# Kernel optimization log

Hardware: AMD Instinct MI355X
Metric: run time of the kernel (lower is better)

The kernel has to match this reference:

```python
import jax, jax.numpy as jnp
import numpy as np

C, V, B, ITERS = 144, 576, 1024, 3  # checks, variables, batch, decoding iterations
COL_W = 4  # variable-node degree (ones per column of H)


def _make_H():
    """Deterministic sparse 0/1 parity-check matrix, col weight COL_W, row weight >= 2."""
    rng = np.random.default_rng(0)
    H = np.zeros((C, V), np.float32)
    for v in range(V):
        H[rng.choice(C, size=COL_W, replace=False), v] = 1.0
    for c in range(C):
        while H[c].sum() < 2:
            H[c, rng.integers(V)] = 1.0
    return H


def setup_inputs() -> dict:
    key = jax.random.key(0)
    r = jax.random.normal(key, (B, V), dtype=jnp.float32)  # channel LLRs, batched
    alpha = 0.7 * jnp.ones((ITERS,), dtype=jnp.float32)    # nn.Parameter init
    H = jnp.asarray(_make_H())                             # [C, V] 0/1 mask
    return {"r": r, "alpha": alpha, "H": H}


def _c_to_v(M, edge, a):
    """Check-to-variable min-sum messages, vectorized over batch and rows.

    For each edge (c,v): E[c,v] = a * (prod of signs of M[c, edges(c)\\{v}])
                                   * (min of |M[c, edges(c)\\{v}]|)
    Implemented with the standard two-smallest-values trick.
    """
    inf = jnp.float32(jnp.inf)
    absM = jnp.where(edge, jnp.abs(M), inf)                 # [B,C,V]
    min1 = jnp.min(absM, axis=-1, keepdims=True)            # smallest |M| per row
    idx = jnp.argmin(absM, axis=-1)                         # [B,C] its position
    is_min = jnp.arange(V)[None, None, :] == idx[..., None]  # one-hot of argmin
    min2 = jnp.min(jnp.where(is_min, inf, absM), axis=-1, keepdims=True)
    excl_min = jnp.where(is_min, min2, min1)                # min excluding self
    sgn = jnp.where(edge, jnp.sign(M), 1.0)
    row_sign = jnp.prod(sgn, axis=-1, keepdims=True)
    sgn_excl = row_sign * sgn                               # product excluding self (signs are +/-1)
    return jnp.where(edge, a * sgn_excl * excl_min, 0.0)


def reference(r, alpha, H):
    edge = (H == 1.0)[None, :, :]                           # [1,C,V] broadcast to batch
    rB = r[:, None, :]                                      # [B,1,V]
    M = jnp.where(edge, rB, 0.0)                            # initial_M: M[c,v]=r[v] on edges
    E = jnp.zeros_like(M)
    for i in range(alpha.shape[0]):
        E = _c_to_v(M, edge, alpha[i])
        col = jnp.sum(E, axis=1, keepdims=True)             # [B,1,V] sum over checks
        M = jnp.where(edge, col - E + rB, 0.0)              # update_M: extrinsic sum + r[v]
    return r + jnp.sum(E, axis=1)                           # [B,V] output LLRs
```

## Files before the change

### kernel.cpp

```cpp
#include <hip/hip_runtime.h>
#include <stdint.h>

#define CN 144
#define VN 576
#define BN 1024
#define NITER 3
#define RCAP 40
#define CCAP 8
#define TPB 192

#define WS_RLEN 0
#define WS_LOC  192
#define WS_CSC  (192 + VN*CN)
#define WS_CCNT (WS_CSC + CCAP*VN)

__device__ __forceinline__ int edge_id(int l, int c) {
    return (((l >> 2) * CN + c) << 2) | (l & 3);
}

__global__ __launch_bounds__(64) void build_stage(const float* __restrict__ H,
                                                  int* __restrict__ ws) {
    const int c = blockIdx.x;
    const int lane = threadIdx.x;
    int base = 0;
    const float* row = H + c * VN;
    for (int ch = 0; ch < VN / 64; ++ch) {
        const int v = ch * 64 + lane;
        const bool set = row[v] > 0.5f;
        const unsigned long long mask = __ballot(set);
        const int off = base + (int)__popcll(mask & ((1ULL << lane) - 1ULL));
        ws[WS_LOC + v * CN + c] = set ? off : -1;
        base += (int)__popcll(mask);
    }
    if (lane == 0) ws[WS_RLEN + c] = base;
}

__global__ __launch_bounds__(64) void build_csc(int* __restrict__ ws) {
    const int v = blockIdx.x;
    const int lane = threadIdx.x;
    int cnt = 0;
    for (int ch = 0; ch < 3; ++ch) {
        const int c = ch * 64 + lane;
        const int l = (c < CN) ? ws[WS_LOC + v * CN + c] : -1;
        const bool set = (l >= 0) && (l < RCAP);
        const unsigned long long mask = __ballot(set);
        const int off = cnt + (int)__popcll(mask & ((1ULL << lane) - 1ULL));
        if (set && off < CCAP) ws[WS_CSC + off * VN + v] = edge_id(l, c);
        cnt += (int)__popcll(mask);
    }
    if (cnt > CCAP) cnt = CCAP;
    if (lane == 0) ws[WS_CCNT + v] = cnt;
    if (lane >= cnt && lane < CCAP) ws[WS_CSC + lane * VN + v] = 0;
}

__global__ __launch_bounds__(TPB) void ldpc_decode(const float* __restrict__ r,
                                                   const float* __restrict__ alpha,
                                                   const int* __restrict__ ws,
                                                   float* __restrict__ out) {
    __shared__ float4 M4[(RCAP / 4) * CN];
    float* const Mf = reinterpret_cast<float*>(M4);

    const int b = blockIdx.x;
    const int t = threadIdx.x;
    const float a_[NITER] = { alpha[0], alpha[1], alpha[2] };

    int   ent4[3][4], entX[3][4];
    int   cnt[3];
    float rv[3];
    #pragma unroll
    for (int q = 0; q < 3; ++q) {
        const int v = t + q * TPB;
        rv[q]  = r[b * VN + v];
        cnt[q] = ws[WS_CCNT + v];
        #pragma unroll
        for (int j = 0; j < 4; ++j) ent4[q][j] = ws[WS_CSC + j * VN + v];
    }
    const int rl = (t < CN) ? ws[WS_RLEN + t] : 0;
    const int any_hi = __syncthreads_or((cnt[0] > 4) | (cnt[1] > 4) | (cnt[2] > 4));
    if (any_hi) {
        #pragma unroll
        for (int q = 0; q < 3; ++q)
            #pragma unroll
            for (int j = 0; j < 4; ++j) entX[q][j] = ws[WS_CSC + (4 + j) * VN + t + q * TPB];
    }

    if (t < CN) {
        const int rpad = (rl + 3) & ~3;
        for (int k = rl; k < rpad; ++k) Mf[edge_id(k, t)] = INFINITY;
    }
    #pragma unroll
    for (int q = 0; q < 3; ++q) {
        #pragma unroll
        for (int j = 0; j < 4; ++j) if (j < cnt[q]) Mf[ent4[q][j]] = rv[q];
    }
    if (any_hi) {
        #pragma unroll
        for (int q = 0; q < 3; ++q) {
            #pragma unroll
            for (int j = 0; j < 4; ++j) if (4 + j < cnt[q]) Mf[entX[q][j]] = rv[q];
        }
    }
    __syncthreads();

    #pragma unroll
    for (int it = 0; it < NITER; ++it) {
        const float a = a_[it];

        if (t < CN) {
            uint32_t m1 = 0x7fffffffu, m2 = 0x7fffffffu, sg = 0u;
            int am = -1;
            const int nq = (rl + 3) >> 2;
            for (int q4 = 0; q4 < nq; ++q4) {
                const float4 mv = M4[q4 * CN + t];
                const float* mvp = reinterpret_cast<const float*>(&mv);
                #pragma unroll
                for (int j = 0; j < 4; ++j) {
                    const uint32_t mb = __float_as_uint(mvp[j]);
                    const uint32_t ab = mb & 0x7fffffffu;
                    sg ^= mb;
                    const bool lt = ab < m1;
                    const uint32_t mn2 = (m2 < ab) ? m2 : ab;
                    m2 = lt ? m1 : mn2;
                    m1 = lt ? ab : m1;
                    am = lt ? (q4 * 4 + j) : am;
                }
            }
            sg &= 0x80000000u;
            const uint32_t p1b = __float_as_uint(a * __uint_as_float(m1)) ^ sg;
            const uint32_t p2b = __float_as_uint(a * __uint_as_float(m2)) ^ sg;

            const int nqf = rl >> 2;
            for (int q4 = 0; q4 < nqf; ++q4) {
                const float4 mv = M4[q4 * CN + t];
                const float* mvp = reinterpret_cast<const float*>(&mv);
                float ev[4];
                #pragma unroll
                for (int j = 0; j < 4; ++j) {
                    const uint32_t mb = __float_as_uint(mvp[j]);
                    const uint32_t ps = ((q4 * 4 + j) == am) ? p2b : p1b;
                    ev[j] = __uint_as_float(ps ^ (mb & 0x80000000u));
                }
                M4[q4 * CN + t] = make_float4(ev[0], ev[1], ev[2], ev[3]);
            }
            if (rl & 3) {
                const int q4 = nqf;
                const float4 mv = M4[q4 * CN + t];
                const float* mvp = reinterpret_cast<const float*>(&mv);
                float ev[4];
                #pragma unroll
                for (int j = 0; j < 4; ++j) {
                    const int k = q4 * 4 + j;
                    const uint32_t mb = __float_as_uint(mvp[j]);
                    const uint32_t ps = (k == am) ? p2b : p1b;
                    ev[j] = (k < rl) ? __uint_as_float(ps ^ (mb & 0x80000000u)) : mvp[j];
                }
                M4[q4 * CN + t] = make_float4(ev[0], ev[1], ev[2], ev[3]);
            }
        }
        __syncthreads();

        #pragma unroll
        for (int q = 0; q < 3; ++q) {
            float E4[4], EX[4];
            float col = 0.0f;
            #pragma unroll
            for (int j = 0; j < 4; ++j) {
                E4[j] = (j < cnt[q]) ? Mf[ent4[q][j]] : 0.0f;
                col += E4[j];
            }
            if (any_hi) {
                #pragma unroll
                for (int j = 0; j < 4; ++j) {
                    EX[j] = (4 + j < cnt[q]) ? Mf[entX[q][j]] : 0.0f;
                    col += EX[j];
                }
            }
            if (it == NITER - 1) {
                out[b * VN + t + q * TPB] = rv[q] + col;
            } else {
                const float mb = col + rv[q];
                #pragma unroll
                for (int j = 0; j < 4; ++j) if (j < cnt[q]) Mf[ent4[q][j]] = mb - E4[j];
                if (any_hi) {
                    #pragma unroll
                    for (int j = 0; j < 4; ++j) if (4 + j < cnt[q]) Mf[entX[q][j]] = mb - EX[j];
                }
            }
        }
        if (it < NITER - 1) __syncthreads();
    }
}

extern "C" void kernel_launch(void* const* d_in, const int* in_sizes, int n_in,
                              void* d_out, int out_size, void* d_ws, size_t ws_size,
                              hipStream_t stream) {
    const float* r     = (const float*)d_in[0];
    const float* alpha = (const float*)d_in[1];
    const float* H     = (const float*)d_in[2];
    float* out = (float*)d_out;
    int* ws    = (int*)d_ws;

    build_stage<<<CN, 64, 0, stream>>>(H, ws);
    build_csc<<<VN, 64, 0, stream>>>(ws);
    ldpc_decode<<<BN, TPB, 0, stream>>>(r, alpha, ws, out);
}
```

Before: 24.86 us.

## Sort check rows by degree, vectorize CSC loads, cache row messages in registers

The last block of build_stage to finish, chosen through an atomic counter, sorts check rows by row length so that adjacent threads in a wavefront have similar loop trip counts. This is meant to reduce divergence in the check-node pass. The CSC edge table is repacked per variable as int4 so each thread reads its entries with one vector load. The check-node pass now keeps the row's float4 messages in registers instead of reading shared memory twice, at the cost of more registers and a fully unrolled, predicated loop.

```diff
diff --git a/kernel.cpp b/kernel.cpp
--- a/kernel.cpp
+++ b/kernel.cpp
@@ -6,33 +6,74 @@
 #define BN 1024
 #define NITER 3
 #define RCAP 40
+#define NQ   (RCAP/4)
 #define CCAP 8
 #define TPB 192
 
 #define WS_RLEN 0
-#define WS_LOC  192
-#define WS_CSC  (192 + VN*CN)
-#define WS_CCNT (WS_CSC + CCAP*VN)
-
-__device__ __forceinline__ int edge_id(int l, int c) {
-    return (((l >> 2) * CN + c) << 2) | (l & 3);
-}
-
-__global__ __launch_bounds__(64) void build_stage(const float* __restrict__ H,
-                                                  int* __restrict__ ws) {
+#define WS_CTR  144
+#define WS_CCOF 160
+#define WS_RLR  304
+#define WS_CCNT 448
+#define WS_LOC  1024
+#define WS_CSC2 (1024 + CN*VN)
+#define WS_CSX  (WS_CSC2 + VN*4)
+
+__device__ __forceinline__ int edge_id(int l, int cc) {
+    return (((l >> 2) * CN + cc) << 2) | (l & 3);
+}
+
+__global__ __launch_bounds__(192) void build_stage(const float* __restrict__ H,
+                                                   int* __restrict__ ws) {
+    __shared__ int rls[CN];
+    __shared__ int hist[RCAP + 1];
+    __shared__ int pfx[RCAP + 1];
+    __shared__ int iswin;
     const int c = blockIdx.x;
-    const int lane = threadIdx.x;
-    int base = 0;
-    const float* row = H + c * VN;
-    for (int ch = 0; ch < VN / 64; ++ch) {
-        const int v = ch * 64 + lane;
-        const bool set = row[v] > 0.5f;
-        const unsigned long long mask = __ballot(set);
-        const int off = base + (int)__popcll(mask & ((1ULL << lane) - 1ULL));
-        ws[WS_LOC + v * CN + c] = set ? off : -1;
-        base += (int)__popcll(mask);
-    }
-    if (lane == 0) ws[WS_RLEN + c] = base;
+    const int t = threadIdx.x;
+
+    if (t < 64) {
+        int base = 0;
+        const float* row = H + c * VN;
+        for (int ch = 0; ch < VN / 64; ++ch) {
+            const int v = ch * 64 + t;
+            const bool set = row[v] > 0.5f;
+            const unsigned long long mask = __ballot(set);
+            const int off = base + (int)__popcll(mask & ((1ULL << t) - 1ULL));
+            ws[WS_LOC + v * CN + c] = set ? off : -1;
+            base += (int)__popcll(mask);
+        }
+        if (t == 0) ws[WS_RLEN + c] = base;
+    }
+    if (t == 0) {
+        __threadfence();
+        const unsigned old = atomicAdd((unsigned*)(ws + WS_CTR), 1u);
+        iswin = ((old % (unsigned)CN) == (unsigned)(CN - 1)) ? 1 : 0;
+    }
+    __syncthreads();
+    if (!iswin) return;
+    __threadfence();
+
+    if (t < CN)
+        rls[t] = min(__hip_atomic_load(ws + WS_RLEN + t, __ATOMIC_RELAXED,
+                                       __HIP_MEMORY_SCOPE_AGENT), RCAP);
+    if (t <= RCAP) hist[t] = 0;
+    __syncthreads();
+    if (t < CN) atomicAdd(&hist[rls[t]], 1);
+    __syncthreads();
+    if (t == 0) {
+        int acc = 0;
+        for (int i = 0; i <= RCAP; ++i) { pfx[i] = acc; acc += hist[i]; }
+    }
+    __syncthreads();
+    if (t < CN) {
+        const int key = rls[t];
+        int tie = 0;
+        for (int c2 = 0; c2 < t; ++c2) tie += (rls[c2] == key) ? 1 : 0;
+        const int cc = pfx[key] + tie;
+        ws[WS_CCOF + t] = cc;
+        ws[WS_RLR + cc] = key;
+    }
 }
 
 __global__ __launch_bounds__(64) void build_csc(int* __restrict__ ws) {
@@ -45,19 +86,25 @@
         const bool set = (l >= 0) && (l < RCAP);
         const unsigned long long mask = __ballot(set);
         const int off = cnt + (int)__popcll(mask & ((1ULL << lane) - 1ULL));
-        if (set && off < CCAP) ws[WS_CSC + off * VN + v] = edge_id(l, c);
+        if (set && off < CCAP) {
+            const int cc = ws[WS_CCOF + c];
+            const int e = edge_id(l, cc);
+            if (off < 4) ws[WS_CSC2 + v * 4 + off] = e;
+            else         ws[WS_CSX  + v * 4 + (off - 4)] = e;
+        }
         cnt += (int)__popcll(mask);
     }
     if (cnt > CCAP) cnt = CCAP;
     if (lane == 0) ws[WS_CCNT + v] = cnt;
-    if (lane >= cnt && lane < CCAP) ws[WS_CSC + lane * VN + v] = 0;
+    if (lane < 4 && lane >= cnt)     ws[WS_CSC2 + v * 4 + lane] = 0;
+    if (lane < 4 && lane + 4 >= cnt) ws[WS_CSX  + v * 4 + lane] = 0;
 }
 
 __global__ __launch_bounds__(TPB) void ldpc_decode(const float* __restrict__ r,
                                                    const float* __restrict__ alpha,
                                                    const int* __restrict__ ws,
                                                    float* __restrict__ out) {
-    __shared__ float4 M4[(RCAP / 4) * CN];
+    __shared__ float4 M4[NQ * CN];
     float* const Mf = reinterpret_cast<float*>(M4);
 
     const int b = blockIdx.x;
@@ -72,16 +119,17 @@
         const int v = t + q * TPB;
         rv[q]  = r[b * VN + v];
         cnt[q] = ws[WS_CCNT + v];
-        #pragma unroll
-        for (int j = 0; j < 4; ++j) ent4[q][j] = ws[WS_CSC + j * VN + v];
-    }
-    const int rl = (t < CN) ? ws[WS_RLEN + t] : 0;
+        const int4 e4 = *reinterpret_cast<const int4*>(ws + WS_CSC2 + v * 4);
+        ent4[q][0] = e4.x; ent4[q][1] = e4.y; ent4[q][2] = e4.z; ent4[q][3] = e4.w;
+    }
+    const int rl = (t < CN) ? ws[WS_RLR + t] : 0;
     const int any_hi = __syncthreads_or((cnt[0] > 4) | (cnt[1] > 4) | (cnt[2] > 4));
     if (any_hi) {
         #pragma unroll
-        for (int q = 0; q < 3; ++q)
-            #pragma unroll
-            for (int j = 0; j < 4; ++j) entX[q][j] = ws[WS_CSC + (4 + j) * VN + t + q * TPB];
+        for (int q = 0; q < 3; ++q) {
+            const int4 e4 = *reinterpret_cast<const int4*>(ws + WS_CSX + (t + q * TPB) * 4);
+            entX[q][0] = e4.x; entX[q][1] = e4.y; entX[q][2] = e4.z; entX[q][3] = e4.w;
+        }
     }
 
     if (t < CN) {
@@ -107,54 +155,46 @@
         const float a = a_[it];
 
         if (t < CN) {
+            const int nq = (rl + 3) >> 2;
+            float4 mv[NQ];
             uint32_t m1 = 0x7fffffffu, m2 = 0x7fffffffu, sg = 0u;
-            int am = -1;
-            const int nq = (rl + 3) >> 2;
-            for (int q4 = 0; q4 < nq; ++q4) {
-                const float4 mv = M4[q4 * CN + t];
-                const float* mvp = reinterpret_cast<const float*>(&mv);
-                #pragma unroll
-                for (int j = 0; j < 4; ++j) {
-                    const uint32_t mb = __float_as_uint(mvp[j]);
-                    const uint32_t ab = mb & 0x7fffffffu;
-                    sg ^= mb;
-                    const bool lt = ab < m1;
-                    const uint32_t mn2 = (m2 < ab) ? m2 : ab;
-                    m2 = lt ? m1 : mn2;
-                    m1 = lt ? ab : m1;
-                    am = lt ? (q4 * 4 + j) : am;
+            int am = 0;
+            #pragma unroll
+            for (int q4 = 0; q4 < NQ; ++q4) {
+                if (q4 < nq) {
+                    mv[q4] = M4[q4 * CN + t];
+                    const float* mp = reinterpret_cast<const float*>(&mv[q4]);
+                    #pragma unroll
+                    for (int j = 0; j < 4; ++j) {
+                        const uint32_t mb = __float_as_uint(mp[j]);
+                        const uint32_t ab = mb & 0x7fffffffu;
+                        sg ^= mb;
+                        const bool lt = ab < m1;
+                        m2 = lt ? m1 : ((ab < m2) ? ab : m2);
+                        m1 = lt ? ab : m1;
+                        am = lt ? (q4 * 4 + j) : am;
+                    }
                 }
             }
             sg &= 0x80000000u;
             const uint32_t p1b = __float_as_uint(a * __uint_as_float(m1)) ^ sg;
             const uint32_t p2b = __float_as_uint(a * __uint_as_float(m2)) ^ sg;
-
-            const int nqf = rl >> 2;
-            for (int q4 = 0; q4 < nqf; ++q4) {
-                const float4 mv = M4[q4 * CN + t];
-                const float* mvp = reinterpret_cast<const float*>(&mv);
-                float ev[4];
-                #pragma unroll
-                for (int j = 0; j < 4; ++j) {
-                    const uint32_t mb = __float_as_uint(mvp[j]);
-                    const uint32_t ps = ((q4 * 4 + j) == am) ? p2b : p1b;
-                    ev[j] = __uint_as_float(ps ^ (mb & 0x80000000u));
-                }
-                M4[q4 * CN + t] = make_float4(ev[0], ev[1], ev[2], ev[3]);
-            }
-            if (rl & 3) {
-                const int q4 = nqf;
-                const float4 mv = M4[q4 * CN + t];
-                const float* mvp = reinterpret_cast<const float*>(&mv);
-                float ev[4];
-                #pragma unroll
-                for (int j = 0; j < 4; ++j) {
-                    const int k = q4 * 4 + j;
-                    const uint32_t mb = __float_as_uint(mvp[j]);
-                    const uint32_t ps = (k == am) ? p2b : p1b;
-                    ev[j] = (k < rl) ? __uint_as_float(ps ^ (mb & 0x80000000u)) : mvp[j];
-                }
-                M4[q4 * CN + t] = make_float4(ev[0], ev[1], ev[2], ev[3]);
+            #pragma unroll
+            for (int q4 = 0; q4 < NQ; ++q4) {
+                if (q4 < nq) {
+                    const float* mp = reinterpret_cast<const float*>(&mv[q4]);
+                    float4 ev;
+                    float* ep = reinterpret_cast<float*>(&ev);
+                    #pragma unroll
+                    for (int j = 0; j < 4; ++j) {
+                        const int k = q4 * 4 + j;
+                        const uint32_t mb = __float_as_uint(mp[j]);
+                        const uint32_t ps = (k == am) ? p2b : p1b;
+                        ep[j] = (k < rl) ? __uint_as_float(ps ^ (mb & 0x80000000u))
+                                         : mp[j];
+                    }
+                    M4[q4 * CN + t] = ev;
+                }
             }
         }
         __syncthreads();
@@ -200,7 +240,7 @@
     float* out = (float*)d_out;
     int* ws    = (int*)d_ws;
 
-    build_stage<<<CN, 64, 0, stream>>>(H, ws);
+    build_stage<<<CN, 192, 0, stream>>>(H, ws);
     build_csc<<<VN, 64, 0, stream>>>(ws);
     ldpc_decode<<<BN, TPB, 0, stream>>>(r, alpha, ws, out);
 }
```

After: 28.48 us. 1.15x slower.

## Process four batch elements per block with float4-interleaved edge messages

Applied to the files above, without the earlier changes.

Each block now decodes four batch rows at once. Each shared-memory float4 holds one edge's messages for the four batch elements, where before it held four consecutive edges of one row. This removes the padding and tail handling and spreads the per-edge index and degree setup over four samples. The cost is 4x shared memory per block (RCAP*CN float4), 4x fewer blocks (256), and RCAP lowered to 32, which could truncate rows with more than 32 edges.

```diff
diff --git a/kernel.cpp b/kernel.cpp
--- a/kernel.cpp
+++ b/kernel.cpp
@@ -5,18 +5,17 @@
 #define VN 576
 #define BN 1024
 #define NITER 3
-#define RCAP 40
+#define RCAP 32
 #define CCAP 8
 #define TPB 192
+#define BPB 4
 
 #define WS_RLEN 0
 #define WS_LOC  192
-#define WS_CSC  (192 + VN*CN)
+#define WS_CSC  (192 + CN*VN)
 #define WS_CCNT (WS_CSC + CCAP*VN)
 
-__device__ __forceinline__ int edge_id(int l, int c) {
-    return (((l >> 2) * CN + c) << 2) | (l & 3);
-}
+union F4 { float4 v; float f[4]; uint32_t u[4]; };
 
 __global__ __launch_bounds__(64) void build_stage(const float* __restrict__ H,
                                                   int* __restrict__ ws) {
@@ -45,7 +44,7 @@
         const bool set = (l >= 0) && (l < RCAP);
         const unsigned long long mask = __ballot(set);
         const int off = cnt + (int)__popcll(mask & ((1ULL << lane) - 1ULL));
-        if (set && off < CCAP) ws[WS_CSC + off * VN + v] = edge_id(l, c);
+        if (set && off < CCAP) ws[WS_CSC + off * VN + v] = l * CN + c;
         cnt += (int)__popcll(mask);
     }
     if (cnt > CCAP) cnt = CCAP;
@@ -53,29 +52,29 @@
     if (lane >= cnt && lane < CCAP) ws[WS_CSC + lane * VN + v] = 0;
 }
 
-__global__ __launch_bounds__(TPB) void ldpc_decode(const float* __restrict__ r,
-                                                   const float* __restrict__ alpha,
-                                                   const int* __restrict__ ws,
-                                                   float* __restrict__ out) {
-    __shared__ float4 M4[(RCAP / 4) * CN];
-    float* const Mf = reinterpret_cast<float*>(M4);
+__global__ __launch_bounds__(TPB) void ldpc_decode4(const float* __restrict__ r,
+                                                    const float* __restrict__ alpha,
+                                                    const int* __restrict__ ws,
+                                                    float* __restrict__ out) {
+    __shared__ float4 M4[RCAP * CN];
 
-    const int b = blockIdx.x;
+    const int b4 = blockIdx.x * BPB;
     const int t = threadIdx.x;
     const float a_[NITER] = { alpha[0], alpha[1], alpha[2] };
 
-    int   ent4[3][4], entX[3][4];
-    int   cnt[3];
-    float rv[3];
+    int ent4[3][4], entX[3][4];
+    int cnt[3];
+    F4  rv[3];
     #pragma unroll
     for (int q = 0; q < 3; ++q) {
         const int v = t + q * TPB;
-        rv[q]  = r[b * VN + v];
+        #pragma unroll
+        for (int s = 0; s < BPB; ++s) rv[q].f[s] = r[(b4 + s) * VN + v];
         cnt[q] = ws[WS_CCNT + v];
         #pragma unroll
         for (int j = 0; j < 4; ++j) ent4[q][j] = ws[WS_CSC + j * VN + v];
     }
-    const int rl = (t < CN) ? ws[WS_RLEN + t] : 0;
+    const int rl = (t < CN) ? min(ws[WS_RLEN + t], RCAP) : 0;
     const int any_hi = __syncthreads_or((cnt[0] > 4) | (cnt[1] > 4) | (cnt[2] > 4));
     if (any_hi) {
         #pragma unroll
@@ -84,20 +83,16 @@
             for (int j = 0; j < 4; ++j) entX[q][j] = ws[WS_CSC + (4 + j) * VN + t + q * TPB];
     }
 
-    if (t < CN) {
-        const int rpad = (rl + 3) & ~3;
-        for (int k = rl; k < rpad; ++k) Mf[edge_id(k, t)] = INFINITY;
-    }
     #pragma unroll
     for (int q = 0; q < 3; ++q) {
         #pragma unroll
-        for (int j = 0; j < 4; ++j) if (j < cnt[q]) Mf[ent4[q][j]] = rv[q];
+        for (int j = 0; j < 4; ++j) if (j < cnt[q]) M4[ent4[q][j]] = rv[q].v;
     }
     if (any_hi) {
         #pragma unroll
         for (int q = 0; q < 3; ++q) {
             #pragma unroll
-            for (int j = 0; j < 4; ++j) if (4 + j < cnt[q]) Mf[entX[q][j]] = rv[q];
+            for (int j = 0; j < 4; ++j) if (4 + j < cnt[q]) M4[entX[q][j]] = rv[q].v;
         }
     }
     __syncthreads();
@@ -107,83 +102,73 @@
         const float a = a_[it];
 
         if (t < CN) {
-            uint32_t m1 = 0x7fffffffu, m2 = 0x7fffffffu, sg = 0u;
-            int am = -1;
-            const int nq = (rl + 3) >> 2;
-            for (int q4 = 0; q4 < nq; ++q4) {
-                const float4 mv = M4[q4 * CN + t];
-                const float* mvp = reinterpret_cast<const float*>(&mv);
+            uint32_t m1[BPB], m2[BPB], sg[BPB]; int am[BPB];
+            #pragma unroll
+            for (int s = 0; s < BPB; ++s) { m1[s] = 0x7fffffffu; m2[s] = 0x7fffffffu; sg[s] = 0u; am[s] = 0; }
+            for (int l = 0; l < rl; ++l) {
+                F4 mv; mv.v = M4[l * CN + t];
                 #pragma unroll
-                for (int j = 0; j < 4; ++j) {
-                    const uint32_t mb = __float_as_uint(mvp[j]);
+                for (int s = 0; s < BPB; ++s) {
+                    const uint32_t mb = mv.u[s];
                     const uint32_t ab = mb & 0x7fffffffu;
-                    sg ^= mb;
-                    const bool lt = ab < m1;
-                    const uint32_t mn2 = (m2 < ab) ? m2 : ab;
-                    m2 = lt ? m1 : mn2;
-                    m1 = lt ? ab : m1;
-                    am = lt ? (q4 * 4 + j) : am;
+                    sg[s] ^= mb;
+                    const bool lt = ab < m1[s];
+                    m2[s] = lt ? m1[s] : ((ab < m2[s]) ? ab : m2[s]);
+                    m1[s] = lt ? ab : m1[s];
+                    am[s] = lt ? l : am[s];
                 }
             }
-            sg &= 0x80000000u;
-            const uint32_t p1b = __float_as_uint(a * __uint_as_float(m1)) ^ sg;
-            const uint32_t p2b = __float_as_uint(a * __uint_as_float(m2)) ^ sg;
-
-            const int nqf = rl >> 2;
-            for (int q4 = 0; q4 < nqf; ++q4) {
-                const float4 mv = M4[q4 * CN + t];
-                const float* mvp = reinterpret_cast<const float*>(&mv);
-                float ev[4];
+            uint32_t p1b[BPB], p2b[BPB];
+            #pragma unroll
+            for (int s = 0; s < BPB; ++s) {
+                const uint32_t sgn = sg[s] & 0x80000000u;
+                p1b[s] = __float_as_uint(a * __uint_as_float(m1[s])) ^ sgn;
+                p2b[s] = __float_as_uint(a * __uint_as_float(m2[s])) ^ sgn;
+            }
+            for (int l = 0; l < rl; ++l) {
+                F4 mv; mv.v = M4[l * CN + t];
+                F4 ev;
                 #pragma unroll
-                for (int j = 0; j < 4; ++j) {
-                    const uint32_t mb = __float_as_uint(mvp[j]);
-                    const uint32_t ps = ((q4 * 4 + j) == am) ? p2b : p1b;
-                    ev[j] = __uint_as_float(ps ^ (mb & 0x80000000u));
+                for (int s = 0; s < BPB; ++s) {
+                    const uint32_t ps = (l == am[s]) ? p2b[s] : p1b[s];
+                    ev.u[s] = ps ^ (mv.u[s] & 0x80000000u);
                 }
-                M4[q4 * CN + t] = make_float4(ev[0], ev[1], ev[2], ev[3]);
-            }
-            if (rl & 3) {
-                const int q4 = nqf;
-                const float4 mv = M4[q4 * CN + t];
-                const float* mvp = reinterpret_cast<const float*>(&mv);
-                float ev[4];
-                #pragma unroll
-                for (int j = 0; j < 4; ++j) {
-                    const int k = q4 * 4 + j;
-                    const uint32_t mb = __float_as_uint(mvp[j]);
-                    const uint32_t ps = (k == am) ? p2b : p1b;
-                    ev[j] = (k < rl) ? __uint_as_float(ps ^ (mb & 0x80000000u)) : mvp[j];
-                }
-                M4[q4 * CN + t] = make_float4(ev[0], ev[1], ev[2], ev[3]);
+                M4[l * CN + t] = ev.v;
             }
         }
         __syncthreads();
 
         #pragma unroll
         for (int q = 0; q < 3; ++q) {
-            float E4[4], EX[4];
-            float col = 0.0f;
+            F4 E4[4], EX[4];
+            F4 col; col.v = make_float4(0.f, 0.f, 0.f, 0.f);
             #pragma unroll
             for (int j = 0; j < 4; ++j) {
-                E4[j] = (j < cnt[q]) ? Mf[ent4[q][j]] : 0.0f;
-                col += E4[j];
+                if (j < cnt[q]) E4[j].v = M4[ent4[q][j]];
+                else            E4[j].v = make_float4(0.f, 0.f, 0.f, 0.f);
+                col.v += E4[j].v;
             }
             if (any_hi) {
                 #pragma unroll
                 for (int j = 0; j < 4; ++j) {
-                    EX[j] = (4 + j < cnt[q]) ? Mf[entX[q][j]] : 0.0f;
-                    col += EX[j];
+                    if (4 + j < cnt[q]) EX[j].v = M4[entX[q][j]];
+                    else                EX[j].v = make_float4(0.f, 0.f, 0.f, 0.f);
+                    col.v += EX[j].v;
                 }
             }
             if (it == NITER - 1) {
-                out[b * VN + t + q * TPB] = rv[q] + col;
+                const int v = t + q * TPB;
+                #pragma unroll
+                for (int s = 0; s < BPB; ++s) out[(b4 + s) * VN + v] = rv[q].f[s] + col.f[s];
             } else {
-                const float mb = col + rv[q];
+                F4 mb; mb.v = col.v + rv[q].v;
                 #pragma unroll
-                for (int j = 0; j < 4; ++j) if (j < cnt[q]) Mf[ent4[q][j]] = mb - E4[j];
+                for (int j = 0; j < 4; ++j)
+                    if (j < cnt[q]) M4[ent4[q][j]] = mb.v - E4[j].v;
                 if (any_hi) {
                     #pragma unroll
-                    for (int j = 0; j < 4; ++j) if (4 + j < cnt[q]) Mf[entX[q][j]] = mb - EX[j];
+                    for (int j = 0; j < 4; ++j)
+                        if (4 + j < cnt[q]) M4[entX[q][j]] = mb.v - EX[j].v;
                 }
             }
         }
@@ -202,5 +187,5 @@
 
     build_stage<<<CN, 64, 0, stream>>>(H, ws);
     build_csc<<<VN, 64, 0, stream>>>(ws);
-    ldpc_decode<<<BN, TPB, 0, stream>>>(r, alpha, ws, out);
+    ldpc_decode4<<<BN / BPB, TPB, 0, stream>>>(r, alpha, ws, out);
 }
```

New measurement: 32.86 us. 32.2% more time.
